# Performance work log

Hardware: AMD Instinct MI355X
Metric: run time of the kernel (lower is better)

The kernel has to match this reference:

```python
import jax, jax.numpy as jnp
import numpy as np

D_MODEL = 1024
N_HEADS = 16
D_K = D_MODEL // N_HEADS
D_FF = 4096
EPS = 1e-5


def _layernorm(x, g, b):
    mu = jnp.mean(x, axis=-1, keepdims=True)
    var = jnp.mean(jnp.square(x - mu), axis=-1, keepdims=True)
    return (x - mu) * jax.lax.rsqrt(var + EPS) * g + b


def setup_inputs() -> dict:
    key = jax.random.key(0)
    ks = jax.random.split(key, 16)
    s = 0.02
    B, S = 2, 2048
    inp = {
        "x": jax.random.normal(ks[0], (B, S, D_MODEL), dtype=jnp.float32),
        "mask": jnp.ones((1, 1, S, S), dtype=jnp.int32),
        # attention projections (stored [in, out]; y = x @ W + b)
        "Wq": jax.random.normal(ks[1], (D_MODEL, D_MODEL)) * s,
        "bq": jnp.zeros((D_MODEL,)),
        "Wk": jax.random.normal(ks[2], (D_MODEL, D_MODEL)) * s,
        "bk": jnp.zeros((D_MODEL,)),
        "Wv": jax.random.normal(ks[3], (D_MODEL, D_MODEL)) * s,
        "bv": jnp.zeros((D_MODEL,)),
        "Wo": jax.random.normal(ks[4], (D_MODEL, D_MODEL)) * s,
        "bo": jnp.zeros((D_MODEL,)),
        "temperature": jnp.sqrt(jnp.array([float(D_K)], dtype=jnp.float32)),
        "time_weights": jax.random.normal(ks[5], (1, N_HEADS, 1, D_K)),
        "gateW": jax.random.normal(ks[6], (D_K, 1)) * s,
        "gateb": jnp.zeros((1,)),
        "ln_attn_g": jnp.ones((D_MODEL,)),
        "ln_attn_b": jnp.zeros((D_MODEL,)),
        # feed-forward
        "fc1W": jax.random.normal(ks[7], (D_MODEL, D_FF)) * s,
        "fc1b": jnp.zeros((D_FF,)),
        "fc2W": jax.random.normal(ks[8], (D_FF, D_MODEL)) * s,
        "fc2b": jnp.zeros((D_MODEL,)),
        "n1g": jnp.ones((D_MODEL,)),
        "n1b": jnp.zeros((D_MODEL,)),
        "n2g": jnp.ones((D_MODEL,)),
        "n2b": jnp.zeros((D_MODEL,)),
    }
    return inp


def reference(x, mask, Wq, bq, Wk, bk, Wv, bv, Wo, bo, temperature,
              time_weights, gateW, gateb, ln_attn_g, ln_attn_b,
              fc1W, fc1b, fc2W, fc2b, n1g, n1b, n2g, n2b):
    B, S, D = x.shape
    H, dk = N_HEADS, D_K

    def heads(t):  # [B,S,D] -> [B,H,S,dk]
        return t.reshape(B, S, H, dk).transpose(0, 2, 1, 3)

    q = heads(x @ Wq + bq) + time_weights  # learned per-head bias on Q
    k = heads(x @ Wk + bk)
    v = heads(x @ Wv + bv)

    scores = jnp.einsum("bhqd,bhkd->bhqk", q, k) / temperature
    scores = jnp.where(mask == 0, jnp.float32(-1e9), scores)
    gate = jax.nn.sigmoid(q @ gateW + gateb)  # [B,H,S,1] per-query gate
    scores = scores * gate
    probs = jax.nn.softmax(scores, axis=-1)

    ctx = jnp.einsum("bhqk,bhkd->bhqd", probs, v)
    ctx = ctx.transpose(0, 2, 1, 3).reshape(B, S, D)
    attn_out = _layernorm(ctx @ Wo + bo, ln_attn_g, ln_attn_b)

    x1 = _layernorm(x + attn_out, n1g, n1b)
    ff = jax.nn.gelu(x1 @ fc1W + fc1b, approximate=False) @ fc2W + fc2b
    return _layernorm(x1 + ff, n2g, n2b)
```

## Files before the change

### kernel.cpp

```cpp
#include <hip/hip_runtime.h>
#include <stdint.h>
#include <math.h>


typedef uint16_t u16;
typedef uint32_t u32;
typedef unsigned long long u64;
typedef __attribute__((ext_vector_type(8))) short short8;
typedef __attribute__((ext_vector_type(4))) float f32x4;

#define S_LEN 2048
#define DM 1024

#define GLOAD_LDS16(g, l)                                                      \
  __builtin_amdgcn_global_load_lds(                                            \
      (const __attribute__((address_space(1))) void*)(g),                      \
      (__attribute__((address_space(3))) void*)(l), 16, 0, 0)

__device__ __forceinline__ float bf2f(u16 h) {
  union { uint32_t u; float f; } x;
  x.u = ((uint32_t)h) << 16;
  return x.f;
}
__device__ __forceinline__ u16 f2bf(float f) {
  union { float f; uint32_t u; } x;
  x.f = f;
  uint32_t r = (x.u + 0x7fffu + ((x.u >> 16) & 1u)) >> 16;
  return (u16)r;
}
__device__ __forceinline__ u16 f2bf_fast(float f) {
  union { float f; uint32_t u; } x;
  x.f = f;
  return (u16)((x.u + 0x8000u) >> 16);
}
__device__ __forceinline__ u32 bfu(float f) {
  union { float f; uint32_t u; } x;
  x.f = f;
  return x.u + 0x8000u;
}

__device__ __forceinline__ float gelu_ex(float v) {
  float x = fabsf(v) * 0.70710678118654752f;
  float t = __builtin_amdgcn_rcpf(__builtin_fmaf(0.3275911f, x, 1.0f));
  float p = 1.061405429f;
  p = __builtin_fmaf(p, t, -1.453152027f);
  p = __builtin_fmaf(p, t, 1.421413741f);
  p = __builtin_fmaf(p, t, -0.284496736f);
  p = __builtin_fmaf(p, t, 0.254829592f);
  p = p * t;
  float ex = __builtin_amdgcn_exp2f(-1.4426950408889634f * x * x);
  float er = __builtin_fmaf(-p, ex, 1.0f);
  er = (v < 0.f) ? -er : er;
  return 0.5f * v * (1.0f + er);
}

union U8 { uint4 u; u16 s[8]; };
union U4 { uint2 u; u16 s[4]; };

__global__ __launch_bounds__(256) void cvt_k(const float* __restrict__ in,
                                             u16* __restrict__ out, int n) {
  int i = (blockIdx.x * 256 + threadIdx.x) * 4;
  if (i >= n) return;
  float4 v = *(const float4*)(in + i);
  U4 o;
  o.s[0] = f2bf(v.x); o.s[1] = f2bf(v.y); o.s[2] = f2bf(v.z); o.s[3] = f2bf(v.w);
  *(uint2*)(out + i) = o.u;
}

__global__ __launch_bounds__(256) void mb_k(const int* __restrict__ mask,
                                            u16* __restrict__ mb) {
  int tid = blockIdx.x * 256 + threadIdx.x;
  const int* src = mask + (size_t)tid * 16;
  uint32_t b = 0;
#pragma unroll
  for (int q = 0; q < 4; q++) {
    int4 m = *(const int4*)(src + q * 4);
    b |= (m.x != 0 ? 1u : 0u) << (q * 4 + 0);
    b |= (m.y != 0 ? 1u : 0u) << (q * 4 + 1);
    b |= (m.z != 0 ? 1u : 0u) << (q * 4 + 2);
    b |= (m.w != 0 ? 1u : 0u) << (q * 4 + 3);
  }
  mb[tid] = (u16)b;
}

__device__ __forceinline__ void tcvt_body(const float* __restrict__ in,
                                          u16* __restrict__ out, int R, int C) {
  __shared__ u16 tile[64][72];
  int c0 = blockIdx.x * 64, r0 = blockIdx.y * 64;
  int t = threadIdx.x;
  int r = t & 63, seg = t >> 6;
  const float* src = in + (size_t)(r0 + r) * C + c0 + seg * 16;
#pragma unroll
  for (int q = 0; q < 4; q++) {
    float4 v = *(const float4*)(src + q * 4);
    tile[r][seg * 16 + q * 4 + 0] = f2bf(v.x);
    tile[r][seg * 16 + q * 4 + 1] = f2bf(v.y);
    tile[r][seg * 16 + q * 4 + 2] = f2bf(v.z);
    tile[r][seg * 16 + q * 4 + 3] = f2bf(v.w);
  }
  __syncthreads();
  U8 v0, v1;
#pragma unroll
  for (int i = 0; i < 8; i++) v0.s[i] = tile[seg * 16 + i][r];
#pragma unroll
  for (int i = 0; i < 8; i++) v1.s[i] = tile[seg * 16 + 8 + i][r];
  u16* dst = out + (size_t)(c0 + r) * R + r0 + seg * 16;
  *(uint4*)dst = v0.u;
  *(uint4*)(dst + 8) = v1.u;
}

__global__ __launch_bounds__(256) void transpose_cvt_k(const float* __restrict__ in,
                                                       u16* __restrict__ out,
                                                       int R, int C) {
  tcvt_body(in, out, R, C);
}

__global__ __launch_bounds__(256) void transpose_cvt3_k(const float* __restrict__ i0,
                                                        const float* __restrict__ i1,
                                                        const float* __restrict__ i2,
                                                        u16* __restrict__ o0,
                                                        u16* __restrict__ o1,
                                                        u16* __restrict__ o2) {
  int z = blockIdx.z;
  const float* in = (z == 0) ? i0 : (z == 1) ? i1 : i2;
  u16* out = (z == 0) ? o0 : (z == 1) ? o1 : o2;
  tcvt_body(in, out, 1024, 1024);
}

__global__ __launch_bounds__(256) void vtrans_k(const u16* __restrict__ V,
                                                u16* __restrict__ VT) {
  __shared__ u16 tile[64][72];
  int bx = blockIdx.x, bh = blockIdx.y;
  int b = bh >> 4, h = bh & 15;
  int t = threadIdx.x, r = t & 63, seg = t >> 6;
  const u16* src = V + (size_t)(b * S_LEN + bx * 64 + r) * DM + h * 64 + seg * 16;
  *(uint4*)&tile[r][seg * 16] = *(const uint4*)src;
  *(uint4*)&tile[r][seg * 16 + 8] = *(const uint4*)(src + 8);
  __syncthreads();
  U8 v0, v1;
#pragma unroll
  for (int i = 0; i < 8; i++) v0.s[i] = tile[seg * 16 + i][r];
#pragma unroll
  for (int i = 0; i < 8; i++) v1.s[i] = tile[seg * 16 + 8 + i][r];
  u16* dst = VT + ((size_t)bh * 64 + r) * S_LEN + bx * 64 + seg * 16;
  *(uint4*)dst = v0.u;
  *(uint4*)(dst + 8) = v1.u;
}

template <int BM, int EPI, int MXS>
__global__ __launch_bounds__(256) void gemm_bt(const u16* __restrict__ A,
                                               const u16* __restrict__ Bt,
                                               u16* __restrict__ C,
                                               const float* __restrict__ bias,
                                               int M, int N, int K) {
  constexpr int MI = BM / 32;
  constexpr int RPW = BM / 4;
  constexpr int AQ = RPW / 16;
  __shared__ u16 As[3 * BM * 32];
  __shared__ u16 Bs[3 * 128 * 32];
  int t = threadIdx.x;
  int wid = t >> 6, lane = t & 63;
  int g = lane >> 4, li = lane & 15;
  int bx = MXS ? blockIdx.y : blockIdx.x;
  int by = MXS ? blockIdx.x : blockIdx.y;
  int wr = (wid >> 1) * (BM / 2), wc = (wid & 1) * 64;

  const u16* a0 = A + (size_t)(by * BM + wid * RPW + (lane >> 2)) * K + (lane & 3) * 8;
  const u16* b0 = Bt + (size_t)(bx * 128 + wid * 32 + (lane >> 2)) * K + (lane & 3) * 8;

  f32x4 acc[MI][4];
#pragma unroll
  for (int i = 0; i < MI; i++)
#pragma unroll
    for (int j = 0; j < 4; j++) acc[i][j] = (f32x4){0.f, 0.f, 0.f, 0.f};

  auto stage = [&](int buf, int kk) {
    u16* la = As + buf * (BM * 32) + wid * RPW * 32;
    u16* lb = Bs + buf * (128 * 32) + wid * 1024;
#pragma unroll
    for (int q = 0; q < AQ; q++)
      GLOAD_LDS16(a0 + (size_t)(q * 16) * K + kk, la + q * 512);
    GLOAD_LDS16(b0 + kk, lb);
    GLOAD_LDS16(b0 + (size_t)16 * K + kk, lb + 512);
  };
  auto compute = [&](int buf) {
    const u16* Ab = As + buf * (BM * 32);
    const u16* Bb = Bs + buf * (128 * 32);
    short8 af[MI], bfv[4];
#pragma unroll
    for (int i = 0; i < MI; i++)
      af[i] = *(const short8*)&Ab[(wr + i * 16 + li) * 32 + g * 8];
#pragma unroll
    for (int i = 0; i < 4; i++)
      bfv[i] = *(const short8*)&Bb[(wc + i * 16 + li) * 32 + g * 8];
    __builtin_amdgcn_s_setprio(1);
#pragma unroll
    for (int mi = 0; mi < MI; mi++)
#pragma unroll
      for (int ni = 0; ni < 4; ni++)
        acc[mi][ni] = __builtin_amdgcn_mfma_f32_16x16x32_bf16(
            af[mi], bfv[ni], acc[mi][ni], 0, 0, 0);
    __builtin_amdgcn_s_setprio(0);
  };

  int n = K >> 5;
  stage(0, 0);
  stage(1, 32);
  int bc = 0, bs = 2;
  for (int ks = 0; ks < n - 1; ks++) {
    if constexpr (AQ == 4)
      asm volatile("s_waitcnt vmcnt(6)" ::: "memory");
    else if constexpr (AQ == 2)
      asm volatile("s_waitcnt vmcnt(4)" ::: "memory");
    else
      asm volatile("s_waitcnt vmcnt(3)" ::: "memory");
    __builtin_amdgcn_s_barrier();
    if (ks + 2 < n) stage(bs, (ks + 2) * 32);
    bs = (bs == 2) ? 0 : bs + 1;
    compute(bc);
    bc = (bc == 2) ? 0 : bc + 1;
  }
  asm volatile("s_waitcnt vmcnt(0)" ::: "memory");
  __builtin_amdgcn_s_barrier();
  compute(bc);

#pragma unroll
  for (int ni = 0; ni < 4; ni++) {
    int col = bx * 128 + wc + ni * 16 + li;
    float bv = bias[col];
#pragma unroll
    for (int mi = 0; mi < MI; mi++) {
#pragma unroll
      for (int r = 0; r < 4; r++) {
        int row = by * BM + wr + mi * 16 + g * 4 + r;
        float v = acc[mi][ni][r] + bv;
        if (EPI == 2) v = gelu_ex(v);
        C[(size_t)row * N + col] = f2bf(v);
      }
    }
  }
}

__global__ __launch_bounds__(256) void qkv_gemm(const u16* __restrict__ A,
                                                const u16* __restrict__ WTq,
                                                const u16* __restrict__ WTk,
                                                const u16* __restrict__ WTv,
                                                u16* __restrict__ Cq,
                                                u16* __restrict__ Ck,
                                                u16* __restrict__ Cv,
                                                const float* __restrict__ bq,
                                                const float* __restrict__ bk,
                                                const float* __restrict__ bv,
                                                const float* __restrict__ tw) {
  const int K = 1024, N = 1024;
  __shared__ u16 As[3 * 128 * 32];
  __shared__ u16 Bs[3 * 128 * 32];
  int t = threadIdx.x;
  int wid = t >> 6, lane = t & 63;
  int g = lane >> 4, li = lane & 15;
  int by = blockIdx.x, bx = blockIdx.y, z = blockIdx.z;
  int wr = (wid >> 1) * 64, wc = (wid & 1) * 64;

  const u16* Bt = (z == 0) ? WTq : (z == 1) ? WTk : WTv;
  u16* C = (z == 0) ? Cq : (z == 1) ? Ck : Cv;
  const float* bias = (z == 0) ? bq : (z == 1) ? bk : bv;

  const u16* a0 = A + (size_t)(by * 128 + wid * 32 + (lane >> 2)) * K + (lane & 3) * 8;
  const u16* b0 = Bt + (size_t)(bx * 128 + wid * 32 + (lane >> 2)) * K + (lane & 3) * 8;

  f32x4 acc[4][4];
#pragma unroll
  for (int i = 0; i < 4; i++)
#pragma unroll
    for (int j = 0; j < 4; j++) acc[i][j] = (f32x4){0.f, 0.f, 0.f, 0.f};

  auto stage = [&](int buf, int kk) {
    u16* la = As + buf * 4096 + wid * 1024;
    u16* lb = Bs + buf * 4096 + wid * 1024;
    GLOAD_LDS16(a0 + kk, la);
    GLOAD_LDS16(a0 + (size_t)16 * K + kk, la + 512);
    GLOAD_LDS16(b0 + kk, lb);
    GLOAD_LDS16(b0 + (size_t)16 * K + kk, lb + 512);
  };
  auto compute = [&](int buf) {
    const u16* Ab = As + buf * 4096;
    const u16* Bb = Bs + buf * 4096;
    short8 af[4], bfv[4];
#pragma unroll
    for (int i = 0; i < 4; i++)
      af[i] = *(const short8*)&Ab[(wr + i * 16 + li) * 32 + g * 8];
#pragma unroll
    for (int i = 0; i < 4; i++)
      bfv[i] = *(const short8*)&Bb[(wc + i * 16 + li) * 32 + g * 8];
    __builtin_amdgcn_s_setprio(1);
#pragma unroll
    for (int mi = 0; mi < 4; mi++)
#pragma unroll
      for (int ni = 0; ni < 4; ni++)
        acc[mi][ni] = __builtin_amdgcn_mfma_f32_16x16x32_bf16(
            af[mi], bfv[ni], acc[mi][ni], 0, 0, 0);
    __builtin_amdgcn_s_setprio(0);
  };

  const int n = 32;
  stage(0, 0);
  stage(1, 32);
  int bc = 0, bs = 2;
  for (int ks = 0; ks < n - 1; ks++) {
    asm volatile("s_waitcnt vmcnt(4)" ::: "memory");
    __builtin_amdgcn_s_barrier();
    if (ks + 2 < n) stage(bs, (ks + 2) * 32);
    bs = (bs == 2) ? 0 : bs + 1;
    compute(bc);
    bc = (bc == 2) ? 0 : bc + 1;
  }
  asm volatile("s_waitcnt vmcnt(0)" ::: "memory");
  __builtin_amdgcn_s_barrier();
  compute(bc);

#pragma unroll
  for (int ni = 0; ni < 4; ni++) {
    int col = bx * 128 + wc + ni * 16 + li;
    float bvv = bias[col];
    if (z == 0) bvv += tw[col];
#pragma unroll
    for (int mi = 0; mi < 4; mi++) {
#pragma unroll
      for (int r = 0; r < 4; r++) {
        int row = by * 128 + wr + mi * 16 + g * 4 + r;
        C[(size_t)row * N + col] = f2bf(acc[mi][ni][r] + bvv);
      }
    }
  }
}

__global__ __launch_bounds__(256) void attn_k(const u16* __restrict__ Q,
                                              const u16* __restrict__ Kp,
                                              const u16* __restrict__ VT,
                                              u16* __restrict__ CTX,
                                              const u16* __restrict__ mb,
                                              const float* __restrict__ gateW,
                                              const float* __restrict__ gateb,
                                              const float* __restrict__ temp) {
  __shared__ u16 Qs[64][72];
  __shared__ u16 Ks[64][72];
  __shared__ u16 Vs[64][72];
  __shared__ u16 Ps[4][16][72];
  __shared__ float gate_s[64];

  int blk = blockIdx.x;
  int bh = blk & 31, qt = blk >> 5;
  int b = bh >> 4, h = bh & 15;
  int t = threadIdx.x, wid = t >> 6, lane = t & 63;
  int g = lane >> 4, li = lane & 15;
  int sq0 = qt * 64;

  const u16* Qb  = Q + ((size_t)b * S_LEN) * DM + h * 64;
  const u16* Kb  = Kp + ((size_t)b * S_LEN) * DM + h * 64;
  const u16* VTb = VT + ((size_t)(b * 16 + h) * 64) * S_LEN;

  {
    int r = t >> 2, cs = (t & 3) * 16;
    const u16* src = Qb + (size_t)(sq0 + r) * DM + cs;
    *(uint4*)&Qs[r][cs] = *(const uint4*)src;
    *(uint4*)&Qs[r][cs + 8] = *(const uint4*)(src + 8);
  }
  __syncthreads();
  {
    int r = t >> 2, cs = (t & 3) * 16;
    U8 q0, q1;
    q0.u = *(const uint4*)&Qs[r][cs];
    q1.u = *(const uint4*)&Qs[r][cs + 8];
    float4 w0 = *(const float4*)(gateW + cs);
    float4 w1 = *(const float4*)(gateW + cs + 4);
    float4 w2 = *(const float4*)(gateW + cs + 8);
    float4 w3 = *(const float4*)(gateW + cs + 12);
    float acc;
    acc  = bf2f(q0.s[0]) * w0.x + bf2f(q0.s[1]) * w0.y +
           bf2f(q0.s[2]) * w0.z + bf2f(q0.s[3]) * w0.w;
    acc += bf2f(q0.s[4]) * w1.x + bf2f(q0.s[5]) * w1.y +
           bf2f(q0.s[6]) * w1.z + bf2f(q0.s[7]) * w1.w;
    acc += bf2f(q1.s[0]) * w2.x + bf2f(q1.s[1]) * w2.y +
           bf2f(q1.s[2]) * w2.z + bf2f(q1.s[3]) * w2.w;
    acc += bf2f(q1.s[4]) * w3.x + bf2f(q1.s[5]) * w3.y +
           bf2f(q1.s[6]) * w3.z + bf2f(q1.s[7]) * w3.w;
    acc += __shfl_xor(acc, 1, 64);
    acc += __shfl_xor(acc, 2, 64);
    if ((t & 3) == 0) gate_s[r] = 1.f / (1.f + __expf(-(acc + gateb[0])));
  }
  __syncthreads();

  const float LOG2E = 1.4426950408889634f;
  float invt2 = LOG2E / temp[0];
  const float NEG2 = -1.0e9f * 1.4426950408889634f;
  short8 qf0 = *(const short8*)&Qs[wid * 16 + li][g * 8];
  short8 qf1 = *(const short8*)&Qs[wid * 16 + li][32 + g * 8];
  int myrow = sq0 + wid * 16 + li;
  float gq = gate_s[wid * 16 + li];
  float gqs = gq * invt2;
  float ng = NEG2 * gq;
  const u16* mbp = mb + (size_t)myrow * 128;

  float psl = 0.f;
  f32x4 o[4];
#pragma unroll
  for (int n = 0; n < 4; n++) o[n] = (f32x4){0.f, 0.f, 0.f, 0.f};

  for (int kt = 0; kt < 32; kt++) {
    __syncthreads();
    {
      int r = t >> 2, cs = (t & 3) * 16;
      const u16* srcK = Kb + (size_t)(kt * 64 + r) * DM + cs;
      *(uint4*)&Ks[r][cs] = *(const uint4*)srcK;
      *(uint4*)&Ks[r][cs + 8] = *(const uint4*)(srcK + 8);
      const u16* srcV = VTb + (size_t)r * S_LEN + kt * 64 + cs;
      *(uint4*)&Vs[r][cs] = *(const uint4*)srcV;
      *(uint4*)&Vs[r][cs + 8] = *(const uint4*)(srcV + 8);
    }
    u64 bits = *(const u64*)(mbp + kt * 4);
    __syncthreads();

    f32x4 sc[4];
#pragma unroll
    for (int ni = 0; ni < 4; ni++) {
      sc[ni] = (f32x4){0.f, 0.f, 0.f, 0.f};
      short8 kf0 = *(const short8*)&Ks[ni * 16 + li][g * 8];
      short8 kf1 = *(const short8*)&Ks[ni * 16 + li][32 + g * 8];
      sc[ni] = __builtin_amdgcn_mfma_f32_16x16x32_bf16(kf0, qf0, sc[ni], 0, 0, 0);
      sc[ni] = __builtin_amdgcn_mfma_f32_16x16x32_bf16(kf1, qf1, sc[ni], 0, 0, 0);
    }

    bool allm = (bits == ~0ull);
    u64 bsh = bits >> (g * 4);
    float pp = 0.f;
#pragma unroll
    for (int ni = 0; ni < 4; ni++) {
      float p0, p1, p2, p3;
      if (__all(allm)) {
        p0 = __builtin_amdgcn_exp2f(sc[ni][0] * gqs);
        p1 = __builtin_amdgcn_exp2f(sc[ni][1] * gqs);
        p2 = __builtin_amdgcn_exp2f(sc[ni][2] * gqs);
        p3 = __builtin_amdgcn_exp2f(sc[ni][3] * gqs);
      } else {
        float s0 = ((bsh >> (ni * 16 + 0)) & 1ull) ? sc[ni][0] * gqs : ng;
        float s1 = ((bsh >> (ni * 16 + 1)) & 1ull) ? sc[ni][1] * gqs : ng;
        float s2 = ((bsh >> (ni * 16 + 2)) & 1ull) ? sc[ni][2] * gqs : ng;
        float s3 = ((bsh >> (ni * 16 + 3)) & 1ull) ? sc[ni][3] * gqs : ng;
        p0 = __builtin_amdgcn_exp2f(s0);
        p1 = __builtin_amdgcn_exp2f(s1);
        p2 = __builtin_amdgcn_exp2f(s2);
        p3 = __builtin_amdgcn_exp2f(s3);
      }
      pp += (p0 + p1) + (p2 + p3);
      u32 lo = (bfu(p0) >> 16) | (bfu(p1) & 0xffff0000u);
      u32 hi = (bfu(p2) >> 16) | (bfu(p3) & 0xffff0000u);
      *(uint2*)&Ps[wid][li][ni * 16 + g * 4] = (uint2){lo, hi};
    }
    psl += pp;

    __builtin_amdgcn_wave_barrier();

    short8 pf0 = *(const short8*)&Ps[wid][li][g * 8];
    short8 pf1 = *(const short8*)&Ps[wid][li][32 + g * 8];
#pragma unroll
    for (int ni = 0; ni < 4; ni++) {
      short8 vf0 = *(const short8*)&Vs[ni * 16 + li][g * 8];
      short8 vf1 = *(const short8*)&Vs[ni * 16 + li][32 + g * 8];
      o[ni] = __builtin_amdgcn_mfma_f32_16x16x32_bf16(pf0, vf0, o[ni], 0, 0, 0);
      o[ni] = __builtin_amdgcn_mfma_f32_16x16x32_bf16(pf1, vf1, o[ni], 0, 0, 0);
    }
  }

  float l = psl;
  l += __shfl_xor(l, 16, 64);
  l += __shfl_xor(l, 32, 64);
  float linvOwn = 1.f / l;
  float linv[4];
#pragma unroll
  for (int r = 0; r < 4; r++)
    linv[r] = __shfl(linvOwn, g * 20 + r, 64);

#pragma unroll
  for (int ni = 0; ni < 4; ni++) {
    int col = h * 64 + ni * 16 + li;
#pragma unroll
    for (int r = 0; r < 4; r++) {
      size_t row = (size_t)b * S_LEN + sq0 + wid * 16 + g * 4 + r;
      CTX[row * DM + col] = f2bf(o[ni][r] * linv[r]);
    }
  }
}

__device__ __forceinline__ void block_sum2(float& a, float& b, float* red, int t) {
#pragma unroll
  for (int off = 32; off > 0; off >>= 1) {
    a += __shfl_xor(a, off, 64);
    b += __shfl_xor(b, off, 64);
  }
  __syncthreads();
  if ((t & 63) == 0) {
    red[(t >> 6) * 2] = a;
    red[(t >> 6) * 2 + 1] = b;
  }
  __syncthreads();
  a = red[0] + red[2] + red[4] + red[6];
  b = red[1] + red[3] + red[5] + red[7];
}

__global__ __launch_bounds__(256) void ln1_k(const u16* __restrict__ po,
                                             const float* __restrict__ x,
                                             const float* __restrict__ g1,
                                             const float* __restrict__ b1,
                                             const float* __restrict__ g2,
                                             const float* __restrict__ b2,
                                             u16* __restrict__ x1) {
  __shared__ float red[8];
  int row = blockIdx.x, t = threadIdx.x;
  size_t base = (size_t)row * 1024 + t * 4;
  U4 pv; pv.u = *(const uint2*)(po + base);
  float v[4];
#pragma unroll
  for (int i = 0; i < 4; i++) v[i] = bf2f(pv.s[i]);
  float s1 = v[0] + v[1] + v[2] + v[3];
  float s2 = v[0]*v[0] + v[1]*v[1] + v[2]*v[2] + v[3]*v[3];
  block_sum2(s1, s2, red, t);
  float mu = s1 * (1.f / 1024.f);
  float rs = rsqrtf(s2 * (1.f / 1024.f) - mu * mu + 1e-5f);
  float4 xv = *(const float4*)(x + base);
  float4 g1v = *(const float4*)(g1 + t * 4);
  float4 b1v = *(const float4*)(b1 + t * 4);
  float w[4];
  w[0] = xv.x + ((v[0] - mu) * rs * g1v.x + b1v.x);
  w[1] = xv.y + ((v[1] - mu) * rs * g1v.y + b1v.y);
  w[2] = xv.z + ((v[2] - mu) * rs * g1v.z + b1v.z);
  w[3] = xv.w + ((v[3] - mu) * rs * g1v.w + b1v.w);
  s1 = w[0] + w[1] + w[2] + w[3];
  s2 = w[0]*w[0] + w[1]*w[1] + w[2]*w[2] + w[3]*w[3];
  block_sum2(s1, s2, red, t);
  mu = s1 * (1.f / 1024.f);
  rs = rsqrtf(s2 * (1.f / 1024.f) - mu * mu + 1e-5f);
  float4 g2v = *(const float4*)(g2 + t * 4);
  float4 b2v = *(const float4*)(b2 + t * 4);
  U4 ov;
  ov.s[0] = f2bf((w[0] - mu) * rs * g2v.x + b2v.x);
  ov.s[1] = f2bf((w[1] - mu) * rs * g2v.y + b2v.y);
  ov.s[2] = f2bf((w[2] - mu) * rs * g2v.z + b2v.z);
  ov.s[3] = f2bf((w[3] - mu) * rs * g2v.w + b2v.w);
  *(uint2*)(x1 + base) = ov.u;
}

__global__ __launch_bounds__(256) void ln2_k(const u16* __restrict__ y,
                                             const u16* __restrict__ x1,
                                             const float* __restrict__ g,
                                             const float* __restrict__ b,
                                             float* __restrict__ out) {
  __shared__ float red[8];
  int row = blockIdx.x, t = threadIdx.x;
  size_t base = (size_t)row * 1024 + t * 4;
  U4 yv; yv.u = *(const uint2*)(y + base);
  U4 xv; xv.u = *(const uint2*)(x1 + base);
  float w[4];
#pragma unroll
  for (int i = 0; i < 4; i++) w[i] = bf2f(yv.s[i]) + bf2f(xv.s[i]);
  float s1 = w[0] + w[1] + w[2] + w[3];
  float s2 = w[0]*w[0] + w[1]*w[1] + w[2]*w[2] + w[3]*w[3];
  block_sum2(s1, s2, red, t);
  float mu = s1 * (1.f / 1024.f);
  float rs = rsqrtf(s2 * (1.f / 1024.f) - mu * mu + 1e-5f);
  float4 gv = *(const float4*)(g + t * 4);
  float4 bv = *(const float4*)(b + t * 4);
  float4 ov;
  ov.x = (w[0] - mu) * rs * gv.x + bv.x;
  ov.y = (w[1] - mu) * rs * gv.y + bv.y;
  ov.z = (w[2] - mu) * rs * gv.z + bv.z;
  ov.w = (w[3] - mu) * rs * gv.w + bv.w;
  *(float4*)(out + base) = ov;
}

extern "C" void kernel_launch(void* const* d_in, const int* in_sizes, int n_in,
                              void* d_out, int out_size, void* d_ws, size_t ws_size,
                              hipStream_t stream) {
  (void)in_sizes; (void)n_in; (void)out_size;
  const float* x    = (const float*)d_in[0];
  const int*   mask = (const int*)d_in[1];
  const float* Wq = (const float*)d_in[2];  const float* bq = (const float*)d_in[3];
  const float* Wk = (const float*)d_in[4];  const float* bk = (const float*)d_in[5];
  const float* Wv = (const float*)d_in[6];  const float* bv = (const float*)d_in[7];
  const float* Wo = (const float*)d_in[8];  const float* bo = (const float*)d_in[9];
  const float* temp = (const float*)d_in[10];
  const float* tw   = (const float*)d_in[11];
  const float* gW   = (const float*)d_in[12]; const float* gb  = (const float*)d_in[13];
  const float* lag  = (const float*)d_in[14]; const float* lab = (const float*)d_in[15];
  const float* f1W  = (const float*)d_in[16]; const float* f1b = (const float*)d_in[17];
  const float* f2W  = (const float*)d_in[18]; const float* f2b = (const float*)d_in[19];
  const float* n1g  = (const float*)d_in[20]; const float* n1b = (const float*)d_in[21];
  const float* n2g  = (const float*)d_in[22]; const float* n2b = (const float*)d_in[23];
  float* out = (float*)d_out;

  u16* ws = (u16*)d_ws;
  const size_t MB4 = (size_t)4096 * 1024;
  u16* s0 = ws;
  u16* s1 = ws + 1 * MB4;
  u16* s2 = ws + 2 * MB4;
  u16* s3 = ws + 3 * MB4;
  u16* s4 = ws + 4 * MB4;
  u16* d0 = (u16*)d_out;
  u16* d1 = d0 + MB4;
  bool bigws = ws_size >= (size_t)9 * 8 * 1024 * 1024;
  u16* Hfull = ws + 5 * MB4;

  dim3 blk(256);
  cvt_k<<<dim3(4096), blk, 0, stream>>>(x, s4, 4096 * 1024);
  transpose_cvt3_k<<<dim3(16, 16, 3), blk, 0, stream>>>(Wq, Wk, Wv, s0, s1, s2);
  qkv_gemm<<<dim3(32, 8, 3), blk, 0, stream>>>(s4, s0, s1, s2, s3, d0, d1,
                                               bq, bk, bv, tw);
  vtrans_k<<<dim3(32, 32), blk, 0, stream>>>(d1, s0);
  mb_k<<<dim3(1024), blk, 0, stream>>>(mask, s1);
  transpose_cvt_k<<<dim3(16, 16), blk, 0, stream>>>(Wo, s4, 1024, 1024);
  attn_k<<<dim3(1024), blk, 0, stream>>>(s3, d0, s0, s2, s1, gW, gb, temp);
  gemm_bt<64, 0, 1><<<dim3(64, 8), blk, 0, stream>>>(s2, s4, d0, bo, 4096, 1024, 1024);
  ln1_k<<<dim3(4096), blk, 0, stream>>>(d0, x, lag, lab, n1g, n1b, s3);
  transpose_cvt_k<<<dim3(64, 16), blk, 0, stream>>>(f1W, s0, 1024, 4096);
  transpose_cvt_k<<<dim3(16, 64), blk, 0, stream>>>(f2W, s1, 4096, 1024);
  if (bigws) {
    gemm_bt<256, 2, 0><<<dim3(32, 16), blk, 0, stream>>>(s3, s0, Hfull, f1b,
                                                         4096, 4096, 1024);
    gemm_bt<64, 0, 0><<<dim3(8, 64), blk, 0, stream>>>(Hfull, s1, s2, f2b,
                                                       4096, 1024, 4096);
  } else {
    for (int i = 0; i < 2; i++) {
      const u16* Ai = s3 + (size_t)i * 2048 * 1024;
      u16* Yi = s2 + (size_t)i * 2048 * 1024;
      gemm_bt<128, 2, 0><<<dim3(32, 16), blk, 0, stream>>>(Ai, s0, d0, f1b,
                                                           2048, 4096, 1024);
      gemm_bt<64, 0, 1><<<dim3(32, 8), blk, 0, stream>>>(d0, s1, Yi, f2b,
                                                         2048, 1024, 4096);
    }
  }
  ln2_k<<<dim3(4096), blk, 0, stream>>>(s2, s3, n2g, n2b, out);
}
```

Baseline: 432.7 us.

## Double-buffer K/V tiles in attention with register prefetch and single barrier

The attention kernel now prefetches the next K and V tiles from global memory into registers while computing on the current tile. It writes them into a second LDS buffer after the PV matmul, and uses one lgkmcnt-wait plus barrier per iteration instead of two syncthreads. To fit the extra K/V buffers, the Q tile and the per-wave P staging share one LDS region. This hides global-load latency behind MFMA and exp work, at the cost of more registers and LDS, which may lower occupancy.

```diff
diff --git a/kernel.cpp b/kernel.cpp
--- a/kernel.cpp
+++ b/kernel.cpp
@@ -16,6 +16,12 @@
   __builtin_amdgcn_global_load_lds(                                            \
       (const __attribute__((address_space(1))) void*)(g),                      \
       (__attribute__((address_space(3))) void*)(l), 16, 0, 0)
+
+#define LGKM_BARRIER()                                                         \
+  do {                                                                         \
+    asm volatile("s_waitcnt lgkmcnt(0)" ::: "memory");                         \
+    __builtin_amdgcn_s_barrier();                                              \
+  } while (0)
 
 __device__ __forceinline__ float bf2f(u16 h) {
   union { uint32_t u; float f; } x;
@@ -342,10 +348,9 @@
                                               const float* __restrict__ gateW,
                                               const float* __restrict__ gateb,
                                               const float* __restrict__ temp) {
-  __shared__ u16 Qs[64][72];
-  __shared__ u16 Ks[64][72];
-  __shared__ u16 Vs[64][72];
-  __shared__ u16 Ps[4][16][72];
+  __shared__ u16 QPs[64 * 72];
+  __shared__ u16 Ks[2][64][72];
+  __shared__ u16 Vs[2][64][72];
   __shared__ float gate_s[64];
 
   int blk = blockIdx.x;
@@ -354,23 +359,22 @@
   int t = threadIdx.x, wid = t >> 6, lane = t & 63;
   int g = lane >> 4, li = lane & 15;
   int sq0 = qt * 64;
+  int rr = t >> 2, cs = (t & 3) * 16;
 
   const u16* Qb  = Q + ((size_t)b * S_LEN) * DM + h * 64;
   const u16* Kb  = Kp + ((size_t)b * S_LEN) * DM + h * 64;
   const u16* VTb = VT + ((size_t)(b * 16 + h) * 64) * S_LEN;
 
   {
-    int r = t >> 2, cs = (t & 3) * 16;
-    const u16* src = Qb + (size_t)(sq0 + r) * DM + cs;
-    *(uint4*)&Qs[r][cs] = *(const uint4*)src;
-    *(uint4*)&Qs[r][cs + 8] = *(const uint4*)(src + 8);
+    const u16* src = Qb + (size_t)(sq0 + rr) * DM + cs;
+    *(uint4*)&QPs[rr * 72 + cs] = *(const uint4*)src;
+    *(uint4*)&QPs[rr * 72 + cs + 8] = *(const uint4*)(src + 8);
   }
   __syncthreads();
   {
-    int r = t >> 2, cs = (t & 3) * 16;
     U8 q0, q1;
-    q0.u = *(const uint4*)&Qs[r][cs];
-    q1.u = *(const uint4*)&Qs[r][cs + 8];
+    q0.u = *(const uint4*)&QPs[rr * 72 + cs];
+    q1.u = *(const uint4*)&QPs[rr * 72 + cs + 8];
     float4 w0 = *(const float4*)(gateW + cs);
     float4 w1 = *(const float4*)(gateW + cs + 4);
     float4 w2 = *(const float4*)(gateW + cs + 8);
@@ -386,46 +390,55 @@
            bf2f(q1.s[6]) * w3.z + bf2f(q1.s[7]) * w3.w;
     acc += __shfl_xor(acc, 1, 64);
     acc += __shfl_xor(acc, 2, 64);
-    if ((t & 3) == 0) gate_s[r] = 1.f / (1.f + __expf(-(acc + gateb[0])));
+    if ((t & 3) == 0) gate_s[rr] = 1.f / (1.f + __expf(-(acc + gateb[0])));
   }
   __syncthreads();
 
   const float LOG2E = 1.4426950408889634f;
   float invt2 = LOG2E / temp[0];
   const float NEG2 = -1.0e9f * 1.4426950408889634f;
-  short8 qf0 = *(const short8*)&Qs[wid * 16 + li][g * 8];
-  short8 qf1 = *(const short8*)&Qs[wid * 16 + li][32 + g * 8];
+  short8 qf0 = *(const short8*)&QPs[(wid * 16 + li) * 72 + g * 8];
+  short8 qf1 = *(const short8*)&QPs[(wid * 16 + li) * 72 + 32 + g * 8];
   int myrow = sq0 + wid * 16 + li;
   float gq = gate_s[wid * 16 + li];
   float gqs = gq * invt2;
   float ng = NEG2 * gq;
   const u16* mbp = mb + (size_t)myrow * 128;
+  u16* Pw = QPs + wid * 16 * 72;
 
   float psl = 0.f;
   f32x4 o[4];
 #pragma unroll
   for (int n = 0; n < 4; n++) o[n] = (f32x4){0.f, 0.f, 0.f, 0.f};
 
+  __syncthreads();
+  {
+    const u16* srcK = Kb + (size_t)rr * DM + cs;
+    *(uint4*)&Ks[0][rr][cs] = *(const uint4*)srcK;
+    *(uint4*)&Ks[0][rr][cs + 8] = *(const uint4*)(srcK + 8);
+    const u16* srcV = VTb + (size_t)rr * S_LEN + cs;
+    *(uint4*)&Vs[0][rr][cs] = *(const uint4*)srcV;
+    *(uint4*)&Vs[0][rr][cs + 8] = *(const uint4*)(srcV + 8);
+  }
+  LGKM_BARRIER();
+
   for (int kt = 0; kt < 32; kt++) {
-    __syncthreads();
-    {
-      int r = t >> 2, cs = (t & 3) * 16;
-      const u16* srcK = Kb + (size_t)(kt * 64 + r) * DM + cs;
-      *(uint4*)&Ks[r][cs] = *(const uint4*)srcK;
-      *(uint4*)&Ks[r][cs + 8] = *(const uint4*)(srcK + 8);
-      const u16* srcV = VTb + (size_t)r * S_LEN + kt * 64 + cs;
-      *(uint4*)&Vs[r][cs] = *(const uint4*)srcV;
-      *(uint4*)&Vs[r][cs + 8] = *(const uint4*)(srcV + 8);
+    int cur = kt & 1;
+    uint4 kxa, kxb, vxa, vxb;
+    if (kt + 1 < 32) {
+      const u16* srcK = Kb + (size_t)((kt + 1) * 64 + rr) * DM + cs;
+      kxa = *(const uint4*)srcK; kxb = *(const uint4*)(srcK + 8);
+      const u16* srcV = VTb + (size_t)rr * S_LEN + (kt + 1) * 64 + cs;
+      vxa = *(const uint4*)srcV; vxb = *(const uint4*)(srcV + 8);
     }
     u64 bits = *(const u64*)(mbp + kt * 4);
-    __syncthreads();
 
     f32x4 sc[4];
 #pragma unroll
     for (int ni = 0; ni < 4; ni++) {
       sc[ni] = (f32x4){0.f, 0.f, 0.f, 0.f};
-      short8 kf0 = *(const short8*)&Ks[ni * 16 + li][g * 8];
-      short8 kf1 = *(const short8*)&Ks[ni * 16 + li][32 + g * 8];
+      short8 kf0 = *(const short8*)&Ks[cur][ni * 16 + li][g * 8];
+      short8 kf1 = *(const short8*)&Ks[cur][ni * 16 + li][32 + g * 8];
       sc[ni] = __builtin_amdgcn_mfma_f32_16x16x32_bf16(kf0, qf0, sc[ni], 0, 0, 0);
       sc[ni] = __builtin_amdgcn_mfma_f32_16x16x32_bf16(kf1, qf1, sc[ni], 0, 0, 0);
     }
@@ -454,20 +467,28 @@
       pp += (p0 + p1) + (p2 + p3);
       u32 lo = (bfu(p0) >> 16) | (bfu(p1) & 0xffff0000u);
       u32 hi = (bfu(p2) >> 16) | (bfu(p3) & 0xffff0000u);
-      *(uint2*)&Ps[wid][li][ni * 16 + g * 4] = (uint2){lo, hi};
+      *(uint2*)&Pw[li * 72 + ni * 16 + g * 4] = (uint2){lo, hi};
     }
     psl += pp;
 
     __builtin_amdgcn_wave_barrier();
 
-    short8 pf0 = *(const short8*)&Ps[wid][li][g * 8];
-    short8 pf1 = *(const short8*)&Ps[wid][li][32 + g * 8];
+    short8 pf0 = *(const short8*)&Pw[li * 72 + g * 8];
+    short8 pf1 = *(const short8*)&Pw[li * 72 + 32 + g * 8];
 #pragma unroll
     for (int ni = 0; ni < 4; ni++) {
-      short8 vf0 = *(const short8*)&Vs[ni * 16 + li][g * 8];
-      short8 vf1 = *(const short8*)&Vs[ni * 16 + li][32 + g * 8];
+      short8 vf0 = *(const short8*)&Vs[cur][ni * 16 + li][g * 8];
+      short8 vf1 = *(const short8*)&Vs[cur][ni * 16 + li][32 + g * 8];
       o[ni] = __builtin_amdgcn_mfma_f32_16x16x32_bf16(pf0, vf0, o[ni], 0, 0, 0);
       o[ni] = __builtin_amdgcn_mfma_f32_16x16x32_bf16(pf1, vf1, o[ni], 0, 0, 0);
+    }
+
+    if (kt + 1 < 32) {
+      *(uint4*)&Ks[cur ^ 1][rr][cs]     = kxa;
+      *(uint4*)&Ks[cur ^ 1][rr][cs + 8] = kxb;
+      *(uint4*)&Vs[cur ^ 1][rr][cs]     = vxa;
+      *(uint4*)&Vs[cur ^ 1][rr][cs + 8] = vxb;
+      LGKM_BARRIER();
     }
   }
 
```

After: 438.2 us. Within noise of the previous version (+1.3%).
